# Kernel tuning notes

Measured on AMD Instinct MI355X. Metric: run time of the kernel, lower is better.

## Reference

```python
import jax, jax.numpy as jnp
import numpy as np

PI = float(np.pi)

def _quantize_angle(theta):
    deg = theta * (180.0 / PI)
    deg = jnp.where(deg < 0, deg + 180.0, deg)
    q = jnp.round(deg / 45.0) * 45.0
    # 180 is treated the same as 0 in the original branch (theta==0 or theta==180)
    return jnp.where(q == 180.0, 0.0, q)

def setup_inputs() -> dict:
    key = jax.random.key(0)
    k1, k2 = jax.random.split(key)
    H, W = 4096, 4096
    img = jax.random.uniform(k1, (1, 1, H, W), dtype=jnp.float32)
    theta = jax.random.normal(k2, (1, 1, H, W), dtype=jnp.float32)  # radians
    return {"img": img, "theta": theta}

def reference(img, theta):
    q = _quantize_angle(theta)

    # value of neighbor at (x+dx, y+dy); borders are masked out afterwards so
    # roll wrap-around never affects the result (interior pixels only).
    def nbr(dx, dy):
        return jnp.roll(img, shift=(-dx, -dy), axis=(2, 3))

    def local_max(dx, dy):
        return (img >= nbr(dx, dy)) & (img >= nbr(-dx, -dy))

    m0 = local_max(0, 1)     # theta == 0 / 180: compare (x, y+-1)
    m45 = local_max(1, 1)    # theta == 45:      compare (x+-1, y+-1)
    m90 = local_max(1, 0)    # theta == 90:      compare (x+-1, y)
    m135 = local_max(1, -1)  # theta == 135:     compare (x+1,y-1),(x-1,y+1)

    mask = jnp.where(q == 0.0, m0,
           jnp.where(q == 45.0, m45,
           jnp.where(q == 90.0, m90, m135)))

    H, W = img.shape[2], img.shape[3]
    interior = jnp.zeros((H, W), dtype=bool).at[1:-1, 1:-1].set(True)
    return jnp.where(mask & interior, img, jnp.zeros_like(img))
```

## Files before the change

kernel.cpp:

```cpp
#include <hip/hip_runtime.h>
#include <math.h>

#define IMG_H 4096
#define IMG_W 4096
#define RPT 8
#define WPR (IMG_W / 256)

typedef float floatx4 __attribute__((ext_vector_type(4)));

__device__ __forceinline__ float nms_px(float t, bool interior,
                                        float uL, float uC, float uR,
                                        float cL, float cC, float cR,
                                        float dL, float dC, float dR) {
    float deg = t * 57.29577951308232f;
    deg = (deg < 0.0f) ? deg + 180.0f : deg;
    const bool is0  = (deg >= -22.5f && deg <= 22.5f) || (deg >= 157.5f && deg <= 202.5f);
    const bool is45 = (deg >  22.5f) && (deg <  67.5f);
    const bool is90 = (deg >= 67.5f) && (deg <= 112.5f);
    const float a = is0 ? cR : (is45 ? dR : (is90 ? dC : dL));
    const float b = is0 ? cL : (is45 ? uL : (is90 ? uC : uR));
    return ((cC >= a) && (cC >= b) && interior) ? cC : 0.0f;
}

__global__ __launch_bounds__(256, 2) void nms_kernel(const float* __restrict__ img,
                                                     const float* __restrict__ theta,
                                                     float* __restrict__ out) {
    const int xcd  = blockIdx.x & 7;
    const int slot = blockIdx.x >> 3;
    const int g    = xcd * 64 + (slot >> 2);
    const int seg  = (slot & 3) * 4 + (threadIdx.x >> 6);
    const int lane = threadIdx.x & 63;

    const int wc = seg << 8;
    const int y4 = wc + (lane << 2);
    const int x0 = g * RPT;

    const bool is_l = (lane == 0);
    const bool is_r = (lane == 63);
    const bool edge_lane = is_l || is_r;
    const int ye = is_l ? (wc > 0 ? wc - 1 : 0)
                        : (wc + 256 < IMG_W ? wc + 256 : IMG_W - 1);

    const bool c0_int = (y4 > 0);
    const bool c3_int = (y4 + 4 < IMG_W);

    floatx4 r[RPT + 2];
    float   e[RPT + 2];
    floatx4 th[RPT];

    #pragma unroll
    for (int i = 0; i < RPT + 2; ++i) {
        int x = x0 - 1 + i;
        x = (x < 0) ? 0 : ((x > IMG_H - 1) ? IMG_H - 1 : x);
        const float* __restrict__ pr = img + (size_t)x * IMG_W;
        r[i] = *(const floatx4*)(pr + y4);
        e[i] = 0.0f;
        if (edge_lane) e[i] = pr[ye];
    }
    #pragma unroll
    for (int i = 0; i < RPT; ++i) {
        const float* tp = theta + (size_t)(x0 + i) * IMG_W + y4;
        th[i] = __builtin_nontemporal_load((const floatx4*)tp);
    }

    #pragma unroll
    for (int i = 0; i < RPT; ++i) {
        const int x = x0 + i;
        const floatx4 u = r[i],   c = r[i + 1], d = r[i + 2];
        const float  ue = e[i],  ce = e[i + 1], de = e[i + 2];
        const floatx4 t = th[i];

        const float uLs = __shfl_up(u.w, 1, 64), uRs = __shfl_down(u.x, 1, 64);
        const float cLs = __shfl_up(c.w, 1, 64), cRs = __shfl_down(c.x, 1, 64);
        const float dLs = __shfl_up(d.w, 1, 64), dRs = __shfl_down(d.x, 1, 64);
        const float uL = is_l ? ue : uLs, uR = is_r ? ue : uRs;
        const float cL = is_l ? ce : cLs, cR = is_r ? ce : cRs;
        const float dL = is_l ? de : dLs, dR = is_r ? de : dRs;

        const bool row_int = (x > 0) && (x < IMG_H - 1);

        floatx4 o;
        o.x = nms_px(t.x, row_int && c0_int, uL,  u.x, u.y,  cL,  c.x, c.y,  dL,  d.x, d.y);
        o.y = nms_px(t.y, row_int,           u.x, u.y, u.z,  c.x, c.y, c.z,  d.x, d.y, d.z);
        o.z = nms_px(t.z, row_int,           u.y, u.z, u.w,  c.y, c.z, c.w,  d.y, d.z, d.w);
        o.w = nms_px(t.w, row_int && c3_int, u.z, u.w, uR,   c.z, c.w, cR,   d.z, d.w, dR);

        floatx4* po = (floatx4*)(out + (size_t)x * IMG_W + y4);
        __builtin_nontemporal_store(o, po);
    }
}

extern "C" void kernel_launch(void* const* d_in, const int* in_sizes, int n_in,
                              void* d_out, int out_size, void* d_ws, size_t ws_size,
                              hipStream_t stream) {
    const float* img   = (const float*)d_in[0];
    const float* theta = (const float*)d_in[1];
    float* out = (float*)d_out;

    const int total_threads = (IMG_H / RPT) * WPR * 64;
    const int block = 256;
    const int grid = total_threads / block;
    nms_kernel<<<grid, block, 0, stream>>>(img, theta, out);
}
```

Measured before the change: 169.6 us.

## Use raw buffer loads with staged waitcnt to overlap first-half compute with loads

Replaces the global loads and stores with inline-asm buffer_load/store instructions built on buffer resource descriptors. Out-of-range rows at the image top and bottom now return zero through the hardware bounds check instead of index clamping. Loads are reordered into two halves, and an explicit s_waitcnt lets the first four rows be computed and stored while the second half's loads are still in flight. The trade-off is that every lane now issues the edge loads, not just the boundary lanes. It also leans on hand-counted vmcnt values that the compiler cannot check.

```diff
diff --git a/kernel.cpp b/kernel.cpp
--- a/kernel.cpp
+++ b/kernel.cpp
@@ -1,5 +1,4 @@
 #include <hip/hip_runtime.h>
-#include <math.h>
 
 #define IMG_H 4096
 #define IMG_W 4096
@@ -7,6 +6,30 @@
 #define WPR (IMG_W / 256)
 
 typedef float floatx4 __attribute__((ext_vector_type(4)));
+typedef int   intx4   __attribute__((ext_vector_type(4)));
+
+__device__ __forceinline__ floatx4 bload4(intx4 rsrc, int voff) {
+    floatx4 d;
+    asm volatile("buffer_load_dwordx4 %0, %1, %2, 0 offen"
+                 : "=v"(d) : "v"(voff), "s"(rsrc));
+    return d;
+}
+__device__ __forceinline__ floatx4 bload4_nt(intx4 rsrc, int voff) {
+    floatx4 d;
+    asm volatile("buffer_load_dwordx4 %0, %1, %2, 0 offen nt"
+                 : "=v"(d) : "v"(voff), "s"(rsrc));
+    return d;
+}
+__device__ __forceinline__ float bload1(intx4 rsrc, int voff) {
+    float d;
+    asm volatile("buffer_load_dword %0, %1, %2, 0 offen"
+                 : "=v"(d) : "v"(voff), "s"(rsrc));
+    return d;
+}
+__device__ __forceinline__ void bstore4_nt(intx4 rsrc, int voff, floatx4 v) {
+    asm volatile("buffer_store_dwordx4 %0, %1, %2, 0 offen nt"
+                 :: "v"(v), "v"(voff), "s"(rsrc) : "memory");
+}
 
 __device__ __forceinline__ float nms_px(float t, bool interior,
                                         float uL, float uC, float uR,
@@ -37,34 +60,56 @@
 
     const bool is_l = (lane == 0);
     const bool is_r = (lane == 63);
-    const bool edge_lane = is_l || is_r;
     const int ye = is_l ? (wc > 0 ? wc - 1 : 0)
                         : (wc + 256 < IMG_W ? wc + 256 : IMG_W - 1);
 
     const bool c0_int = (y4 > 0);
     const bool c3_int = (y4 + 4 < IMG_W);
 
+    intx4 rimg, rth, rout;
+    rimg.x = (int)(uintptr_t)img;
+    rimg.y = (int)(((uintptr_t)img) >> 32) & 0xFFFF;
+    rimg.z = IMG_H * IMG_W * 4;
+    rimg.w = 0x00020000;
+    rth.x  = (int)(uintptr_t)theta;
+    rth.y  = (int)(((uintptr_t)theta) >> 32) & 0xFFFF;
+    rth.z  = IMG_H * IMG_W * 4;
+    rth.w  = 0x00020000;
+    rout.x = (int)(uintptr_t)out;
+    rout.y = (int)(((uintptr_t)out) >> 32) & 0xFFFF;
+    rout.z = IMG_H * IMG_W * 4;
+    rout.w = 0x00020000;
+
     floatx4 r[RPT + 2];
     float   e[RPT + 2];
     floatx4 th[RPT];
 
+    const int rowb  = IMG_W * 4;
+    const int base  = (x0 - 1) * rowb + y4 * 4;
+    const int ebase = (x0 - 1) * rowb + ye * 4;
+
     #pragma unroll
-    for (int i = 0; i < RPT + 2; ++i) {
-        int x = x0 - 1 + i;
-        x = (x < 0) ? 0 : ((x > IMG_H - 1) ? IMG_H - 1 : x);
-        const float* __restrict__ pr = img + (size_t)x * IMG_W;
-        r[i] = *(const floatx4*)(pr + y4);
-        e[i] = 0.0f;
-        if (edge_lane) e[i] = pr[ye];
+    for (int i = 0; i < 4; ++i)
+        th[i] = bload4_nt(rth, (x0 + i) * rowb + y4 * 4);
+    #pragma unroll
+    for (int k = 0; k < 6; ++k) {
+        r[k] = bload4(rimg, base + k * rowb);
+        e[k] = bload1(rimg, ebase + k * rowb);
     }
     #pragma unroll
-    for (int i = 0; i < RPT; ++i) {
-        const float* tp = theta + (size_t)(x0 + i) * IMG_W + y4;
-        th[i] = __builtin_nontemporal_load((const floatx4*)tp);
+    for (int i = 4; i < 8; ++i)
+        th[i] = bload4_nt(rth, (x0 + i) * rowb + y4 * 4);
+    #pragma unroll
+    for (int k = 6; k < 10; ++k) {
+        r[k] = bload4(rimg, base + k * rowb);
+        e[k] = bload1(rimg, ebase + k * rowb);
     }
 
+    asm volatile("s_waitcnt vmcnt(12)" ::: "memory");
+    __builtin_amdgcn_sched_barrier(0);
+
     #pragma unroll
-    for (int i = 0; i < RPT; ++i) {
+    for (int i = 0; i < 4; ++i) {
         const int x = x0 + i;
         const floatx4 u = r[i],   c = r[i + 1], d = r[i + 2];
         const float  ue = e[i],  ce = e[i + 1], de = e[i + 2];
@@ -85,8 +130,35 @@
         o.z = nms_px(t.z, row_int,           u.y, u.z, u.w,  c.y, c.z, c.w,  d.y, d.z, d.w);
         o.w = nms_px(t.w, row_int && c3_int, u.z, u.w, uR,   c.z, c.w, cR,   d.z, d.w, dR);
 
-        floatx4* po = (floatx4*)(out + (size_t)x * IMG_W + y4);
-        __builtin_nontemporal_store(o, po);
+        bstore4_nt(rout, x * rowb + y4 * 4, o);
+    }
+
+    asm volatile("s_waitcnt vmcnt(4)" ::: "memory");
+    __builtin_amdgcn_sched_barrier(0);
+
+    #pragma unroll
+    for (int i = 4; i < 8; ++i) {
+        const int x = x0 + i;
+        const floatx4 u = r[i],   c = r[i + 1], d = r[i + 2];
+        const float  ue = e[i],  ce = e[i + 1], de = e[i + 2];
+        const floatx4 t = th[i];
+
+        const float uLs = __shfl_up(u.w, 1, 64), uRs = __shfl_down(u.x, 1, 64);
+        const float cLs = __shfl_up(c.w, 1, 64), cRs = __shfl_down(c.x, 1, 64);
+        const float dLs = __shfl_up(d.w, 1, 64), dRs = __shfl_down(d.x, 1, 64);
+        const float uL = is_l ? ue : uLs, uR = is_r ? ue : uRs;
+        const float cL = is_l ? ce : cLs, cR = is_r ? ce : cRs;
+        const float dL = is_l ? de : dLs, dR = is_r ? de : dRs;
+
+        const bool row_int = (x > 0) && (x < IMG_H - 1);
+
+        floatx4 o;
+        o.x = nms_px(t.x, row_int && c0_int, uL,  u.x, u.y,  cL,  c.x, c.y,  dL,  d.x, d.y);
+        o.y = nms_px(t.y, row_int,           u.x, u.y, u.z,  c.x, c.y, c.z,  d.x, d.y, d.z);
+        o.z = nms_px(t.z, row_int,           u.y, u.z, u.w,  c.y, c.z, c.w,  d.y, d.z, d.w);
+        o.w = nms_px(t.w, row_int && c3_int, u.z, u.w, uR,   c.z, c.w, cR,   d.z, d.w, dR);
+
+        bstore4_nt(rout, x * rowb + y4 * 4, o);
     }
 }
 
```

After: 168.0 us. Within noise of the previous version (-0.9%).
